# Optimization experiments

Measured on AMD Instinct MI355X. Metric: run time of the kernel, lower is better.

## Reference

```python
import jax, jax.numpy as jnp
import numpy as np
from jax.scipy.special import erf

N_GRAPHS, N_PER, C, NB, NEL = 64, 256, 64, 8, 10
DEG = 24
R_MAX = 5.0
P_CUT = 5
AVG_NEIGH = 24.0
SIGMA = 1.0  # atomic_multipoles_smearing_width
L_IDX = jnp.array([0, 1, 1, 1, 2, 2, 2, 2, 2])  # irrep index of each of the 9 sh components


def _sph(v):
    # real spherical harmonics up to l=2, e3nn 'component' normalization, unit input
    x, y, z = v[:, 0], v[:, 1], v[:, 2]
    s3, s15, s5 = 3.0 ** 0.5, 15.0 ** 0.5, 5.0 ** 0.5
    return jnp.stack([
        jnp.ones_like(x),
        s3 * x, s3 * y, s3 * z,
        s15 * x * y, s15 * y * z, 0.5 * s5 * (3.0 * z * z - 1.0),
        s15 * x * z, 0.5 * s15 * (x * x - y * y),
    ], axis=-1)


def _radial(r):
    # Bessel basis * polynomial cutoff envelope (MACE RadialEmbeddingBlock)
    x = r / R_MAX
    p = float(P_CUT)
    env = (1.0 - 0.5 * (p + 1.0) * (p + 2.0) * x ** P_CUT
           + p * (p + 2.0) * x ** (P_CUT + 1)
           - 0.5 * p * (p + 1.0) * x ** (P_CUT + 2))
    env = jnp.where(x < 1.0, env, 0.0)
    n = jnp.arange(1, NB + 1, dtype=r.dtype)
    bess = jnp.sqrt(2.0 / R_MAX) * jnp.sin(n * jnp.pi * x[:, None]) / jnp.clip(r, 1e-9)[:, None]
    return bess * env[:, None]


def setup_inputs() -> dict:
    rng = np.random.default_rng(0)
    N = N_GRAPHS * N_PER
    z = rng.integers(0, NEL, N)
    node_attrs = jnp.asarray(np.eye(NEL, dtype=np.float32)[z])
    pos = rng.uniform(0.0, 8.0, (N, 3)).astype(np.float32)
    positions = jnp.asarray(pos)
    # edges within each graph (no self loops)
    src = rng.integers(0, N_PER, (N_GRAPHS, N_PER * DEG))
    dst = (src + 1 + rng.integers(0, N_PER - 1, (N_GRAPHS, N_PER * DEG))) % N_PER
    off = (np.arange(N_GRAPHS) * N_PER)[:, None]
    edge_index = jnp.asarray(np.stack([(src + off).reshape(-1), (dst + off).reshape(-1)]).astype(np.int64))
    batch = jnp.asarray(np.repeat(np.arange(N_GRAPHS), N_PER).astype(np.int64))
    key = jax.random.key(0)
    ks = jax.random.split(key, 14)
    p = lambda k, shape, s: jax.random.normal(k, shape, jnp.float32) * s
    return dict(
        node_attrs=node_attrs, positions=positions, edge_index=edge_index, batch=batch,
        W_embed=p(ks[0], (NEL, C), 0.3), E0=p(ks[1], (NEL,), 1.0),
        rW1=p(ks[2], (2, NB, 64), 0.3), rW2=p(ks[3], (2, 64, 64), 0.15),
        rW3=p(ks[4], (2, 64, 64), 0.15), rW4=p(ks[5], (2, 64, C), 0.15),
        Wmix=p(ks[6], (2, 3, C, C), 0.1), Wsc=p(ks[7], (2, NEL, C), 0.3),
        w2=p(ks[8], (2, NEL, C), 0.1), w3=p(ks[9], (2, NEL, C), 0.05),
        Wr0=p(ks[10], (C,), 0.1), Wh=p(ks[11], (C, 16), 0.2),
        Wo=p(ks[12], (16,), 0.2), Wq=p(ks[13], (2, C), 0.05),
    )


def reference(node_attrs, positions, edge_index, batch, W_embed, E0, rW1, rW2, rW3, rW4,
              Wmix, Wsc, w2, w3, Wr0, Wh, Wo, Wq):
    N = node_attrs.shape[0]
    src, dst = edge_index[0], edge_index[1]
    # edge vectors / lengths / spherical harmonics / radial features
    vec = positions[dst] - positions[src]                       # [E,3]
    r = jnp.linalg.norm(vec, axis=-1)
    unit = vec / jnp.clip(r, 1e-9)[:, None]
    sh = _sph(unit)                                             # [E,9]
    ef = _radial(r)                                             # [E,NB]
    # node embedding (scalar channel only populated)
    feats = jnp.zeros((N, C, 9), node_attrs.dtype)
    feats = feats.at[:, :, 0].set(node_attrs @ W_embed)
    node_e0 = node_attrs @ E0                                   # [N]
    e0 = jax.ops.segment_sum(node_e0, batch, num_segments=N_GRAPHS)
    energies, node_es = [e0], [node_e0]
    q = jnp.zeros((N,), node_attrs.dtype)
    silu = jax.nn.silu
    for t in range(2):
        # radial MLP -> per-edge, per-channel weights
        R = silu(silu(silu(ef @ rW1[t]) @ rW2[t]) @ rW3[t]) @ rW4[t]   # [E,C]
        s_src = feats[src, :, 0]                                       # [E,C] gather
        msg = (s_src * R)[:, :, None] * sh[:, None, :]                 # [E,C,9]
        agg = jax.ops.segment_sum(msg, dst, num_segments=N) / AVG_NEIGH  # [N,C,9] scatter
        # per-l linear channel mixing
        mixed = jnp.einsum('ncm,mdc->ndm', agg, Wmix[t][L_IDX])        # [N,C,9]
        # correlation-order product basis (element-dependent, up to correlation 3)
        g2 = node_attrs @ w2[t]
        g3 = node_attrs @ w3[t]
        s = mixed[:, :, 0]
        prodf = mixed + (g2 * s)[:, :, None] * mixed + (g3 * s * s)[:, :, None] * mixed
        # element-dependent skip connection
        sc = feats * (node_attrs @ Wsc[t])[:, :, None]
        feats = prodf + sc
        # readout (nonlinear MLP on last layer)
        if t == 1:
            ne = silu(feats[:, :, 0] @ Wh) @ Wo
        else:
            ne = feats[:, :, 0] @ Wr0
        energies.append(jax.ops.segment_sum(ne, batch, num_segments=N_GRAPHS))
        node_es.append(ne)
        # environment-dependent charge source (max_l = 0 -> monopole)
        q = q + feats[:, :, 0] @ Wq[t]
    contributions = jnp.stack(energies, axis=-1)                # [G, L+1]
    total_energy = contributions.sum(-1)
    node_energy = jnp.stack(node_es, axis=-1).sum(-1)
    # direct (PBC-agnostic) Gaussian-smeared Coulomb, per graph
    qg = q.reshape(N_GRAPHS, N_PER)
    pg = positions.reshape(N_GRAPHS, N_PER, 3)
    d = pg[:, :, None, :] - pg[:, None, :, :]
    rij = jnp.sqrt((d * d).sum(-1) + 1e-12)
    ker = erf(rij / (2.0 * SIGMA)) / rij
    ker = jnp.where(jnp.eye(N_PER, dtype=bool)[None], 0.0, ker)  # no self interaction
    ecoul = 0.5 * jnp.einsum('gi,gij,gj->g', qg, ker, qg)
    total_energy = total_energy + ecoul
    dipole = jnp.einsum('gi,gix->gx', qg, pg)                   # [G,3]
    return total_energy, node_energy, contributions, q, dipole
```

## Files before the change

kernel.cpp:

```cpp
#include <hip/hip_runtime.h>
#include <math.h>

#define NGRAPH 64
#define NPER   256
#define NNODE  (NGRAPH*NPER)
#define CDIM   64
#define NELEM  10
#define NEDGE  (NNODE*24)
#define RMAX2  25.0f

typedef _Float16 half8 __attribute__((ext_vector_type(8)));
typedef float floatx4 __attribute__((ext_vector_type(4)));

__device__ __forceinline__ float silu_f(float x){ return x/(1.f+__expf(-x)); }

__global__ __launch_bounds__(256) void k_pw(
    const float* __restrict__ rW1, const float* __restrict__ rW2,
    const float* __restrict__ rW3, const float* __restrict__ rW4,
    const float* __restrict__ Wmix, _Float16* __restrict__ wH, _Float16* __restrict__ wmixH)
{
  int t = blockIdx.x;
  int tid = threadIdx.x, w = tid>>6, ln = tid&63, ln15 = ln&15, quad = ln>>4;
  const float* Ws[4] = {rW1 + t*512, rW2 + t*4096, rW3 + t*4096, rW4 + t*4096};
  _Float16* wHt    = wH    + (size_t)t*28*512;
  _Float16* wmixHt = wmixH + (size_t)t*24*512;
  for (int f = w; f < 28; f += 4){
    int l, kt, nt;
    if (f < 4){ l = 0; kt = 0; nt = f; }
    else { int g = f-4; l = 1 + g/8; int r8 = g&7; nt = r8>>1; kt = r8&1; }
    const float* Wp = Ws[l];
    half8 v;
    #pragma unroll
    for (int j = 0; j < 8; j++){
      int k = kt*32 + quad*8 + j;
      int c = nt*16 + ln15;
      float x = (l == 0) ? ((k < 8) ? Wp[k*64+c] : 0.f) : Wp[k*64+c];
      v[j] = (_Float16)x;
    }
    *(half8*)&wHt[((size_t)f*64 + ln)*8] = v;
  }
  const float* Wm = Wmix + (size_t)t*3*4096;
  for (int f = w; f < 24; f += 4){
    int l = f>>3, kt = (f>>2)&1, nt = f&3;
    const float* p = Wm + (size_t)l*4096 + (nt*16+ln15)*64 + kt*32 + quad*8;
    half8 v;
    #pragma unroll
    for (int j = 0; j < 8; j++) v[j] = (_Float16)p[j];
    *(half8*)&wmixHt[((size_t)f*64 + ln)*8] = v;
  }
}

__global__ __launch_bounds__(256) void k_prep(
    const float* __restrict__ attrs, const float* __restrict__ E0,
    int* __restrict__ zidx, float* __restrict__ out_ne, float* __restrict__ out_ctr)
{
  __shared__ float red[4];
  int g = blockIdx.x, tid = threadIdx.x, n = g*256 + tid;
  int z = 0;
  #pragma unroll
  for (int k = 1; k < NELEM; k++) if (attrs[n*NELEM+k] > 0.5f) z = k;
  zidx[n] = z;
  float ev = E0[z];
  out_ne[n] = ev;
  float v = ev;
  #pragma unroll
  for (int o = 32; o > 0; o >>= 1) v += __shfl_down(v, o, 64);
  if ((tid&63) == 0) red[tid>>6] = v;
  __syncthreads();
  if (tid == 0) out_ctr[g*3] = red[0]+red[1]+red[2]+red[3];
}

__global__ __launch_bounds__(256) void k_emb(
    const int* __restrict__ zidx, const float* __restrict__ W_embed, _Float16* __restrict__ sH)
{
  int idx = blockIdx.x*256 + threadIdx.x;
  int n = idx >> 6, c = idx & 63;
  sH[idx] = (_Float16)W_embed[zidx[n]*CDIM + c];
}

__global__ __launch_bounds__(256) void k_count(
    const int* __restrict__ ei, const float* __restrict__ pos, int* __restrict__ deg)
{
  int e = blockIdx.x*256 + threadIdx.x;
  int s = ei[e], d = ei[NEDGE+e];
  float vx = pos[d*3]-pos[s*3], vy = pos[d*3+1]-pos[s*3+1], vz = pos[d*3+2]-pos[s*3+2];
  if (vx*vx+vy*vy+vz*vz < RMAX2) atomicAdd(&deg[d], 1);
}

__global__ __launch_bounds__(1024) void k_scan(const int* __restrict__ deg, int* __restrict__ offs)
{
  __shared__ int sums[1024];
  int t = threadIdx.x;
  int loc[16];
  int s = 0, base = t*16;
  #pragma unroll
  for (int i = 0; i < 16; i++){ loc[i] = s; s += deg[base+i]; }
  sums[t] = s;
  __syncthreads();
  for (int off = 1; off < 1024; off <<= 1){
    int v = (t >= off) ? sums[t-off] : 0;
    __syncthreads();
    sums[t] += v;
    __syncthreads();
  }
  int pre = (t > 0) ? sums[t-1] : 0;
  #pragma unroll
  for (int i = 0; i < 16; i++) offs[base+i] = pre + loc[i];
  if (t == 1023) offs[NNODE] = pre + s;
}

__global__ __launch_bounds__(256) void k_fill(
    const int* __restrict__ ei, const float* __restrict__ pos,
    const int* __restrict__ offs, int* __restrict__ cursor,
    int* __restrict__ srcC, _Float16* __restrict__ efH, _Float16* __restrict__ shH)
{
  int e = blockIdx.x*256 + threadIdx.x;
  int s = ei[e], d = ei[NEDGE+e];
  float vx = pos[d*3]-pos[s*3], vy = pos[d*3+1]-pos[s*3+1], vz = pos[d*3+2]-pos[s*3+2];
  float r2 = vx*vx+vy*vy+vz*vz;
  if (r2 >= RMAX2) return;
  int p = atomicAdd(&cursor[d], 1);
  int slot = offs[d] + p;
  srcC[slot] = s;
  float r = sqrtf(r2);
  float inv = 1.f/fmaxf(r, 1e-9f);
  float x_ = vx*inv, y_ = vy*inv, z_ = vz*inv;
  const float s3 = 1.7320508075688772f, s15 = 3.872983346207417f, s5 = 2.2360679774997896f;
  half8 sv0, sv1;
  sv0[0] = (_Float16)1.f;
  sv0[1] = (_Float16)(s3*x_); sv0[2] = (_Float16)(s3*y_); sv0[3] = (_Float16)(s3*z_);
  sv0[4] = (_Float16)(s15*x_*y_); sv0[5] = (_Float16)(s15*y_*z_);
  sv0[6] = (_Float16)(0.5f*s5*(3.f*z_*z_-1.f)); sv0[7] = (_Float16)(s15*x_*z_);
  #pragma unroll
  for (int j = 0; j < 8; j++) sv1[j] = (_Float16)0.f;
  sv1[0] = (_Float16)(0.5f*s15*(x_*x_-y_*y_));
  *(half8*)&shH[(size_t)slot*16]     = sv0;
  *(half8*)&shH[(size_t)slot*16 + 8] = sv1;
  float xx = r*0.2f;
  float x2 = xx*xx;
  float x5 = x2*x2*xx;
  float env = 1.f - 21.f*x5 + 35.f*x5*xx - 15.f*x5*x2;
  float pref = 0.6324555320336759f*inv*env;
  const float PI_ = 3.14159265358979323846f;
  half8 ev, z8;
  #pragma unroll
  for (int b = 0; b < 8; b++) ev[b] = (_Float16)(pref*sinf((float)(b+1)*PI_*xx));
  #pragma unroll
  for (int j = 0; j < 8; j++) z8[j] = (_Float16)0.f;
  _Float16* efp = efH + (size_t)slot*32;
  *(half8*)&efp[0]  = ev;
  *(half8*)&efp[8]  = z8;
  *(half8*)&efp[16] = z8;
  *(half8*)&efp[24] = z8;
}

__global__ __launch_bounds__(256) void k_R(
    const _Float16* __restrict__ efH, const int* __restrict__ srcC,
    const _Float16* __restrict__ sH, const int* __restrict__ nact_p,
    const _Float16* __restrict__ wHt, _Float16* __restrict__ RCh)
{
  __shared__ __align__(16) _Float16 hS[64*72];
  __shared__ int srcS[64];
  int nact = *nact_p;
  int ebase = blockIdx.x*64;
  if (ebase >= nact) return;
  int tid = threadIdx.x;
  int w = tid>>6, ln = tid&63, ln15 = ln&15, quad = ln>>4;

  half8 bL1 = *(const half8*)&wHt[((size_t)(0 + w)*64 + ln)*8];
  half8 bf[3][2];
  #pragma unroll
  for (int l = 0; l < 3; l++){
    bf[l][0] = *(const half8*)&wHt[((size_t)(4 + l*8 + w*2 + 0)*64 + ln)*8];
    bf[l][1] = *(const half8*)&wHt[((size_t)(4 + l*8 + w*2 + 1)*64 + ln)*8];
  }
  if (tid < 64){
    int idx = ebase + tid; if (idx > nact-1) idx = nact-1;
    srcS[tid] = srcC[idx];
  }

  floatx4 zero = {0.f, 0.f, 0.f, 0.f};
  floatx4 acc[4];

  #pragma unroll
  for (int mt = 0; mt < 4; mt++){
    int idx = ebase + mt*16 + ln15; if (idx > nact-1) idx = nact-1;
    half8 a = *(const half8*)&efH[(size_t)idx*32 + quad*8];
    acc[mt] = __builtin_amdgcn_mfma_f32_16x16x32_f16(a, bL1, zero, 0, 0, 0);
  }
  #pragma unroll
  for (int mt = 0; mt < 4; mt++)
    #pragma unroll
    for (int r = 0; r < 4; r++)
      hS[(mt*16 + quad*4 + r)*72 + w*16 + ln15] = (_Float16)silu_f(acc[mt][r]);
  __syncthreads();

  float sv[16];
  #pragma unroll
  for (int mt = 0; mt < 4; mt++)
    #pragma unroll
    for (int r = 0; r < 4; r++){
      int el = mt*16 + quad*4 + r;
      sv[mt*4+r] = (float)sH[(size_t)srcS[el]*64 + w*16 + ln15];
    }

  #pragma unroll
  for (int l = 0; l < 3; l++){
    #pragma unroll
    for (int mt = 0; mt < 4; mt++){
      half8 a0 = *(const half8*)&hS[(mt*16 + ln15)*72 + quad*8];
      half8 a1 = *(const half8*)&hS[(mt*16 + ln15)*72 + 32 + quad*8];
      floatx4 t0 = __builtin_amdgcn_mfma_f32_16x16x32_f16(a0, bf[l][0], zero, 0, 0, 0);
      acc[mt] = __builtin_amdgcn_mfma_f32_16x16x32_f16(a1, bf[l][1], t0, 0, 0, 0);
    }
    __syncthreads();
    if (l < 2){
      #pragma unroll
      for (int mt = 0; mt < 4; mt++)
        #pragma unroll
        for (int r = 0; r < 4; r++)
          hS[(mt*16 + quad*4 + r)*72 + w*16 + ln15] = (_Float16)silu_f(acc[mt][r]);
      __syncthreads();
    }
  }

  #pragma unroll
  for (int mt = 0; mt < 4; mt++)
    #pragma unroll
    for (int r = 0; r < 4; r++){
      int el = mt*16 + quad*4 + r;
      int idx = ebase + el; if (idx > nact-1) idx = nact-1;
      RCh[(size_t)idx*64 + w*16 + ln15] = (_Float16)(acc[mt][r] * sv[mt*4+r]);
    }
}

__global__ __launch_bounds__(256) void k_am(
    const _Float16* __restrict__ RCh, const _Float16* __restrict__ shH,
    const int* __restrict__ offs, const _Float16* __restrict__ sH,
    _Float16* __restrict__ feats1, const _Float16* __restrict__ wmixHt,
    const int* __restrict__ zidx,
    const float* __restrict__ Wsc_t, const float* __restrict__ w2_t,
    const float* __restrict__ w3_t, const float* __restrict__ Wq_t,
    const float* __restrict__ Wr0, const float* __restrict__ Wh, const float* __restrict__ Wo,
    float* __restrict__ out_ne, float* __restrict__ out_ctr, float* __restrict__ out_q, int t)
{
  __shared__ __align__(16) _Float16 aggS[9*16*72];
  __shared__ float tabS[3*640];
  __shared__ float WhS[1024];
  __shared__ _Float16 f0S[16*64];
  __shared__ float qS[4][16], neS[4][16];
  __shared__ float WqS[64], Wr0S[64], WoS[16];
  __shared__ int zS[16];

  int blk = blockIdx.x;
  int tid = threadIdx.x;
  int w = tid>>6, ln = tid&63, ln15 = ln&15, quad = ln>>4;

  for (int i = tid; i < 1920; i += 256){
    int t3 = i/640, rem = i - t3*640;
    const float* src = (t3 == 0) ? Wsc_t : (t3 == 1) ? w2_t : w3_t;
    tabS[i] = src[rem];
  }
  for (int i = tid; i < 1024; i += 256) WhS[i] = Wh[i];
  if (tid < 64){ WqS[tid] = Wq_t[tid]; Wr0S[tid] = Wr0[tid]; }
  if (tid < 16){ WoS[tid] = Wo[tid]; zS[tid] = zidx[blk*16+tid]; }

  #pragma unroll
  for (int i = 0; i < 4; i++){
    int nl = w*4 + i;
    int n = blk*16 + nl;
    int beg = offs[n], end = offs[n+1];
    float acc[9] = {0,0,0,0,0,0,0,0,0};
    for (int p = beg; p < end; ++p){
      float rc = (float)RCh[(size_t)p*64 + ln];
      const _Float16* sp = shH + (size_t)p*16;
      half8 s0 = *(const half8*)sp;
      half8 s1 = *(const half8*)(sp+8);
      acc[0] += rc*(float)s0[0]; acc[1] += rc*(float)s0[1];
      acc[2] += rc*(float)s0[2]; acc[3] += rc*(float)s0[3];
      acc[4] += rc*(float)s0[4]; acc[5] += rc*(float)s0[5];
      acc[6] += rc*(float)s0[6]; acc[7] += rc*(float)s0[7];
      acc[8] += rc*(float)s1[0];
    }
    #pragma unroll
    for (int m = 0; m < 9; m++)
      aggS[(m*16 + nl)*72 + ln] = (_Float16)(acc[m]*(1.f/24.f));
  }
  __syncthreads();

  floatx4 zero = {0.f, 0.f, 0.f, 0.f};
  floatx4 acc[9];
  #pragma unroll
  for (int m = 0; m < 9; m++){
    int l = (m == 0) ? 0 : ((m < 4) ? 1 : 2);
    half8 a0 = *(const half8*)&aggS[(m*16 + ln15)*72 + quad*8];
    half8 a1 = *(const half8*)&aggS[(m*16 + ln15)*72 + 32 + quad*8];
    half8 b0 = *(const half8*)&wmixHt[((size_t)(l*8 + w)*64 + ln)*8];
    half8 b1 = *(const half8*)&wmixHt[((size_t)(l*8 + 4 + w)*64 + ln)*8];
    floatx4 t0 = __builtin_amdgcn_mfma_f32_16x16x32_f16(a0, b0, zero, 0, 0, 0);
    acc[m] = __builtin_amdgcn_mfma_f32_16x16x32_f16(a1, b1, t0, 0, 0, 0);
  }

  int d = w*16 + ln15;
  #pragma unroll
  for (int r = 0; r < 4; r++){
    int nl = quad*4 + r;
    size_t nglob = (size_t)blk*16 + nl;
    int z = zS[nl];
    float wsc = tabS[z*64+d];
    float g2  = tabS[640 + z*64+d];
    float g3  = tabS[1280 + z*64+d];
    float s0 = acc[0][r];
    float factor = 1.f + g2*s0 + g3*s0*s0;
    float f0 = 0.f;
    #pragma unroll
    for (int m = 0; m < 9; m++){
      float fold;
      if (t == 0) fold = (m == 0) ? (float)sH[nglob*64 + d] : 0.f;
      else        fold = (float)feats1[((size_t)m*NNODE + nglob)*64 + d];
      float fnew = acc[m][r]*factor + fold*wsc;
      if (t == 0) feats1[((size_t)m*NNODE + nglob)*64 + d] = (_Float16)fnew;
      if (m == 0) f0 = fnew;
    }
    if (t == 1) f0S[nl*64 + d] = (_Float16)f0;
    float qv = f0*WqS[d];
    float nev = (t == 0) ? f0*Wr0S[d] : 0.f;
    #pragma unroll
    for (int o = 1; o < 16; o <<= 1){
      qv  += __shfl_xor(qv, o, 16);
      nev += __shfl_xor(nev, o, 16);
    }
    if (ln15 == 0){ qS[w][nl] = qv; neS[w][nl] = nev; }
  }
  __syncthreads();

  if (w == 0 && ln < 16){
    float q = qS[0][ln]+qS[1][ln]+qS[2][ln]+qS[3][ln];
    out_q[blk*16+ln] += q;
    if (t == 0){
      float ne = neS[0][ln]+neS[1][ln]+neS[2][ln]+neS[3][ln];
      out_ne[blk*16+ln] += ne;
      neS[0][ln] = ne;
    }
  }
  if (t == 1 && w == 1){
    int iloc = ln>>4, j = ln&15;
    #pragma unroll
    for (int it = 0; it < 4; it++){
      int i = it*4 + iloc;
      float h = 0.f;
      #pragma unroll 8
      for (int dd = 0; dd < 64; dd++) h += (float)f0S[i*64+dd]*WhS[dd*16+j];
      h = silu_f(h)*WoS[j];
      #pragma unroll
      for (int o = 1; o < 16; o <<= 1) h += __shfl_xor(h, o, 16);
      if (j == 0){ neS[0][i] = h; out_ne[blk*16+i] += h; }
    }
  }
  __syncthreads();
  if (tid == 0){
    float s = 0.f;
    #pragma unroll
    for (int i = 0; i < 16; i++) s += neS[0][i];
    atomicAdd(&out_ctr[(blk>>4)*3 + 1 + t], s);
  }
}

__global__ __launch_bounds__(256) void k_coul(
    const float* __restrict__ q, const float* __restrict__ pos,
    float* __restrict__ te, float* __restrict__ dip)
{
  __shared__ float qs[256], px[256], py[256], pz[256];
  int g = blockIdx.x >> 4, rt = blockIdx.x & 15;
  int tid = threadIdx.x;
  int base = g*256;
  qs[tid] = q[base+tid];
  px[tid] = pos[(base+tid)*3];
  py[tid] = pos[(base+tid)*3+1];
  pz[tid] = pos[(base+tid)*3+2];
  __syncthreads();
  int rloc = rt*16 + (tid>>4);
  int jc = tid & 15;
  float qi = qs[rloc], xi = px[rloc], yi = py[rloc], zi = pz[rloc];
  float srow = 0.f;
  #pragma unroll
  for (int u = 0; u < 16; u++){
    int j = jc*16 + u;
    float dx = xi-px[j], dy = yi-py[j], dz = zi-pz[j];
    float r = sqrtf(dx*dx+dy*dy+dz*dz + 1e-12f);
    float v = erff(0.5f*r)/r;
    srow += (j == rloc) ? 0.f : qs[j]*v;
  }
  #pragma unroll
  for (int o = 8; o > 0; o >>= 1) srow += __shfl_xor(srow, o, 16);
  float vals[4] = {0.f, 0.f, 0.f, 0.f};
  if (jc == 0){ vals[0] = 0.5f*qi*srow; vals[1] = qi*xi; vals[2] = qi*yi; vals[3] = qi*zi; }
  #pragma unroll
  for (int k = 0; k < 4; k++){
    #pragma unroll
    for (int o = 32; o > 0; o >>= 1) vals[k] += __shfl_down(vals[k], o, 64);
  }
  if ((tid&63) == 0){
    atomicAdd(&te[g], vals[0]);
    atomicAdd(&dip[g*3+0], vals[1]);
    atomicAdd(&dip[g*3+1], vals[2]);
    atomicAdd(&dip[g*3+2], vals[3]);
  }
}

__global__ __launch_bounds__(64) void k_fin(const float* __restrict__ ctr, float* __restrict__ te)
{
  int g = threadIdx.x;
  te[g] += ctr[g*3] + ctr[g*3+1] + ctr[g*3+2];
}

extern "C" void kernel_launch(void* const* d_in, const int* in_sizes, int n_in,
                              void* d_out, int out_size, void* d_ws, size_t ws_size,
                              hipStream_t stream)
{
  (void)in_sizes; (void)n_in; (void)out_size; (void)ws_size;
  const float* attrs   = (const float*)d_in[0];
  const float* pos     = (const float*)d_in[1];
  const int*   ei      = (const int*)d_in[2];
  const float* W_embed = (const float*)d_in[4];
  const float* E0      = (const float*)d_in[5];
  const float* rW1     = (const float*)d_in[6];
  const float* rW2     = (const float*)d_in[7];
  const float* rW3     = (const float*)d_in[8];
  const float* rW4     = (const float*)d_in[9];
  const float* Wmix    = (const float*)d_in[10];
  const float* Wsc     = (const float*)d_in[11];
  const float* w2      = (const float*)d_in[12];
  const float* w3      = (const float*)d_in[13];
  const float* Wr0     = (const float*)d_in[14];
  const float* Wh      = (const float*)d_in[15];
  const float* Wo      = (const float*)d_in[16];
  const float* Wq      = (const float*)d_in[17];

  char* base = (char*)d_ws;
  _Float16* efH   = (_Float16*)base; base += (size_t)NEDGE*32*2;
  _Float16* shH   = (_Float16*)base; base += (size_t)NEDGE*16*2;
  _Float16* RCh   = (_Float16*)base; base += (size_t)NEDGE*64*2;
  _Float16* sH    = (_Float16*)base; base += (size_t)NNODE*64*2;
  _Float16* feats1= (_Float16*)base; base += (size_t)9*NNODE*64*2;
  _Float16* wH    = (_Float16*)base; base += (size_t)2*28*512*2;
  _Float16* wmixH = (_Float16*)base; base += (size_t)2*24*512*2;
  int*      deg   = (int*)base;      base += (size_t)NNODE*4;
  int*      offs  = (int*)base;      base += (size_t)(NNODE+1)*4;
  int*      cursor= (int*)base;      base += (size_t)NNODE*4;
  int*      srcC  = (int*)base;      base += (size_t)NEDGE*4;
  int*      zidx  = (int*)base;      base += (size_t)NNODE*4;

  float* out_te  = (float*)d_out;
  float* out_ne  = out_te  + NGRAPH;
  float* out_ctr = out_ne  + NNODE;
  float* out_q   = out_ctr + NGRAPH*3;
  float* out_dip = out_q   + NNODE;

  hipMemsetAsync(d_out, 0, sizeof(float)*(size_t)(NGRAPH + NNODE + NGRAPH*3 + NNODE + NGRAPH*3), stream);
  hipMemsetAsync(deg, 0, sizeof(int)*(size_t)NNODE, stream);
  hipMemsetAsync(cursor, 0, sizeof(int)*(size_t)NNODE, stream);

  k_pw   <<<2, 256, 0, stream>>>(rW1, rW2, rW3, rW4, Wmix, wH, wmixH);
  k_prep <<<NGRAPH, 256, 0, stream>>>(attrs, E0, zidx, out_ne, out_ctr);
  k_emb  <<<NNODE*64/256, 256, 0, stream>>>(zidx, W_embed, sH);
  k_count<<<NEDGE/256, 256, 0, stream>>>(ei, pos, deg);
  k_scan <<<1, 1024, 0, stream>>>(deg, offs);
  k_fill <<<NEDGE/256, 256, 0, stream>>>(ei, pos, offs, cursor, srcC, efH, shH);

  for (int t = 0; t < 2; t++){
    const _Float16* scur = t ? feats1 : sH;
    k_R <<<NEDGE/64, 256, 0, stream>>>(efH, srcC, scur, offs+NNODE,
        wH + (size_t)t*28*512, RCh);
    k_am<<<NNODE/16, 256, 0, stream>>>(RCh, shH, offs, sH, feats1,
        wmixH + (size_t)t*24*512, zidx,
        Wsc + t*NELEM*CDIM, w2 + t*NELEM*CDIM, w3 + t*NELEM*CDIM, Wq + t*CDIM,
        Wr0, Wh, Wo, out_ne, out_ctr, out_q, t);
  }
  k_coul<<<NGRAPH*16, 256, 0, stream>>>(out_q, pos, out_te, out_dip);
  k_fin <<<1, 64, 0, stream>>>(out_ctr, out_te);
}
```

Baseline: 315.5 us.

## Stage block's edge RC and SH chunks in LDS before per-node aggregation

The k_am aggregation loop now cooperatively copies contiguous chunks of the block's edge radial coefficients and spherical harmonics into shared memory with vector loads, then each wave accumulates its four nodes from LDS. This replaces per-lane scattered global reads with coalesced block-wide loads. To fit the staging buffer, weight tables (Wsc/w2/w3 and Wh) are stored in LDS as fp16, lowering their precision, and the agg buffer aliases the staging area. The chunk loop adds extra barriers per chunk.

```diff
diff --git a/kernel.cpp b/kernel.cpp
--- a/kernel.cpp
+++ b/kernel.cpp
@@ -8,6 +8,7 @@
 #define NELEM  10
 #define NEDGE  (NNODE*24)
 #define RMAX2  25.0f
+#define CE     160
 
 typedef _Float16 half8 __attribute__((ext_vector_type(8)));
 typedef float floatx4 __attribute__((ext_vector_type(4)));
@@ -244,13 +245,16 @@
     const float* __restrict__ Wr0, const float* __restrict__ Wh, const float* __restrict__ Wo,
     float* __restrict__ out_ne, float* __restrict__ out_ctr, float* __restrict__ out_q, int t)
 {
-  __shared__ __align__(16) _Float16 aggS[9*16*72];
-  __shared__ float tabS[3*640];
-  __shared__ float WhS[1024];
+  __shared__ __align__(16) _Float16 uni[CE*80];
+  __shared__ _Float16 tabS[1920];
+  __shared__ _Float16 WhS[1024];
   __shared__ _Float16 f0S[16*64];
   __shared__ float qS[4][16], neS[4][16];
   __shared__ float WqS[64], Wr0S[64], WoS[16];
   __shared__ int zS[16];
+  _Float16* stR = uni;
+  _Float16* stS = uni + CE*64;
+  _Float16* aggS = uni;
 
   int blk = blockIdx.x;
   int tid = threadIdx.x;
@@ -259,37 +263,63 @@
   for (int i = tid; i < 1920; i += 256){
     int t3 = i/640, rem = i - t3*640;
     const float* src = (t3 == 0) ? Wsc_t : (t3 == 1) ? w2_t : w3_t;
-    tabS[i] = src[rem];
-  }
-  for (int i = tid; i < 1024; i += 256) WhS[i] = Wh[i];
+    tabS[i] = (_Float16)src[rem];
+  }
+  for (int i = tid; i < 1024; i += 256) WhS[i] = (_Float16)Wh[i];
   if (tid < 64){ WqS[tid] = Wq_t[tid]; Wr0S[tid] = Wr0[tid]; }
   if (tid < 16){ WoS[tid] = Wo[tid]; zS[tid] = zidx[blk*16+tid]; }
 
+  int beg = offs[blk*16], end = offs[blk*16+16];
+  int nb[4], ne_[4];
+  #pragma unroll
+  for (int i = 0; i < 4; i++){
+    nb[i]  = offs[blk*16 + w*4 + i];
+    ne_[i] = offs[blk*16 + w*4 + i + 1];
+  }
+
+  float acc[4][9];
+  #pragma unroll
+  for (int i = 0; i < 4; i++)
+    #pragma unroll
+    for (int m = 0; m < 9; m++) acc[i][m] = 0.f;
+
+  for (int c0 = beg; c0 < end; c0 += CE){
+    int ce = end - c0; if (ce > CE) ce = CE;
+    __syncthreads();
+    for (int i = tid; i < ce*8; i += 256)
+      *(half8*)&stR[i*8] = *(const half8*)&RCh[(size_t)c0*64 + i*8];
+    for (int i = tid; i < ce*2; i += 256)
+      *(half8*)&stS[i*8] = *(const half8*)&shH[(size_t)c0*16 + i*8];
+    __syncthreads();
+    #pragma unroll
+    for (int i = 0; i < 4; i++){
+      int pb = nb[i] > c0 ? nb[i] : c0;
+      int pe = ne_[i] < c0+ce ? ne_[i] : c0+ce;
+      for (int p = pb - c0; p < pe - c0; ++p){
+        float rc = (float)stR[p*64 + ln];
+        const _Float16* sp = &stS[p*16];
+        half8 s0 = *(const half8*)sp;
+        float s8 = (float)sp[8];
+        acc[i][0] += rc*(float)s0[0]; acc[i][1] += rc*(float)s0[1];
+        acc[i][2] += rc*(float)s0[2]; acc[i][3] += rc*(float)s0[3];
+        acc[i][4] += rc*(float)s0[4]; acc[i][5] += rc*(float)s0[5];
+        acc[i][6] += rc*(float)s0[6]; acc[i][7] += rc*(float)s0[7];
+        acc[i][8] += rc*s8;
+      }
+    }
+  }
+  __syncthreads();
   #pragma unroll
   for (int i = 0; i < 4; i++){
     int nl = w*4 + i;
-    int n = blk*16 + nl;
-    int beg = offs[n], end = offs[n+1];
-    float acc[9] = {0,0,0,0,0,0,0,0,0};
-    for (int p = beg; p < end; ++p){
-      float rc = (float)RCh[(size_t)p*64 + ln];
-      const _Float16* sp = shH + (size_t)p*16;
-      half8 s0 = *(const half8*)sp;
-      half8 s1 = *(const half8*)(sp+8);
-      acc[0] += rc*(float)s0[0]; acc[1] += rc*(float)s0[1];
-      acc[2] += rc*(float)s0[2]; acc[3] += rc*(float)s0[3];
-      acc[4] += rc*(float)s0[4]; acc[5] += rc*(float)s0[5];
-      acc[6] += rc*(float)s0[6]; acc[7] += rc*(float)s0[7];
-      acc[8] += rc*(float)s1[0];
-    }
     #pragma unroll
     for (int m = 0; m < 9; m++)
-      aggS[(m*16 + nl)*72 + ln] = (_Float16)(acc[m]*(1.f/24.f));
+      aggS[(m*16 + nl)*72 + ln] = (_Float16)(acc[i][m]*(1.f/24.f));
   }
   __syncthreads();
 
   floatx4 zero = {0.f, 0.f, 0.f, 0.f};
-  floatx4 acc[9];
+  floatx4 macc[9];
   #pragma unroll
   for (int m = 0; m < 9; m++){
     int l = (m == 0) ? 0 : ((m < 4) ? 1 : 2);
@@ -298,7 +328,7 @@
     half8 b0 = *(const half8*)&wmixHt[((size_t)(l*8 + w)*64 + ln)*8];
     half8 b1 = *(const half8*)&wmixHt[((size_t)(l*8 + 4 + w)*64 + ln)*8];
     floatx4 t0 = __builtin_amdgcn_mfma_f32_16x16x32_f16(a0, b0, zero, 0, 0, 0);
-    acc[m] = __builtin_amdgcn_mfma_f32_16x16x32_f16(a1, b1, t0, 0, 0, 0);
+    macc[m] = __builtin_amdgcn_mfma_f32_16x16x32_f16(a1, b1, t0, 0, 0, 0);
   }
 
   int d = w*16 + ln15;
@@ -307,10 +337,10 @@
     int nl = quad*4 + r;
     size_t nglob = (size_t)blk*16 + nl;
     int z = zS[nl];
-    float wsc = tabS[z*64+d];
-    float g2  = tabS[640 + z*64+d];
-    float g3  = tabS[1280 + z*64+d];
-    float s0 = acc[0][r];
+    float wsc = (float)tabS[z*64+d];
+    float g2  = (float)tabS[640 + z*64+d];
+    float g3  = (float)tabS[1280 + z*64+d];
+    float s0 = macc[0][r];
     float factor = 1.f + g2*s0 + g3*s0*s0;
     float f0 = 0.f;
     #pragma unroll
@@ -318,7 +348,7 @@
       float fold;
       if (t == 0) fold = (m == 0) ? (float)sH[nglob*64 + d] : 0.f;
       else        fold = (float)feats1[((size_t)m*NNODE + nglob)*64 + d];
-      float fnew = acc[m][r]*factor + fold*wsc;
+      float fnew = macc[m][r]*factor + fold*wsc;
       if (t == 0) feats1[((size_t)m*NNODE + nglob)*64 + d] = (_Float16)fnew;
       if (m == 0) f0 = fnew;
     }
@@ -350,7 +380,7 @@
       int i = it*4 + iloc;
       float h = 0.f;
       #pragma unroll 8
-      for (int dd = 0; dd < 64; dd++) h += (float)f0S[i*64+dd]*WhS[dd*16+j];
+      for (int dd = 0; dd < 64; dd++) h += (float)f0S[i*64+dd]*(float)WhS[dd*16+j];
       h = silu_f(h)*WoS[j];
       #pragma unroll
       for (int o = 1; o < 16; o <<= 1) h += __shfl_xor(h, o, 16);
```

New measurement: 295.6 us. 1.07x faster.
